# Kernel tuning notes

Hardware: AMD Instinct MI355X
Metric: run time of the kernel (lower is better)

## Reference

```python
import jax, jax.numpy as jnp
import numpy as np

N = 100000          # nodes
E = 1600000         # edges (avg degree 16)
DIN = 64
DOUT = 64
EXPERTS = 3
GATE_C = 4
TEMP = 101.0        # batch=0 < decay_lim: 100 - 0 + final_temperature(1.0)


def setup_inputs() -> dict:
    key = jax.random.key(0)
    ks = jax.random.split(key, 6)
    x = jax.random.normal(ks[0], (N, DIN), dtype=jnp.float32)
    edge_index = jax.random.randint(ks[1], (2, E), 0, N, dtype=jnp.int32)
    gate_features = jax.random.normal(ks[2], (N, GATE_C), dtype=jnp.float32)
    # per-expert GCN linear weights/bias (PyG GCNConv: lin then bias)
    W = jax.random.normal(ks[3], (EXPERTS, DIN, DOUT), dtype=jnp.float32) / np.sqrt(DIN).astype(np.float32)
    b = jnp.zeros((EXPERTS, DOUT), dtype=jnp.float32)
    # gating nn.Linear(gate_channels, experts, bias=False); stored as [GATE_C, EXPERTS] so y = gf @ Wg
    Wg = jax.random.normal(ks[4], (GATE_C, EXPERTS), dtype=jnp.float32) / np.sqrt(GATE_C).astype(np.float32)
    return {"x": x, "edge_index": edge_index, "gate_features": gate_features,
            "W": W, "b": b, "Wg": Wg}


def reference(x, edge_index, gate_features, W, b, Wg):
    n = x.shape[0]
    # --- GCN normalization with self-loops (PyG GCNConv defaults) ---
    loops = jnp.arange(n, dtype=edge_index.dtype)
    rows = jnp.concatenate([edge_index[0], loops])   # source nodes, [E+N]
    cols = jnp.concatenate([edge_index[1], loops])   # target nodes, [E+N]
    deg = jax.ops.segment_sum(jnp.ones(rows.shape, dtype=x.dtype), cols, num_segments=n)
    dinv = jnp.where(deg > 0, jax.lax.rsqrt(deg), 0.0)
    norm = dinv[rows] * dinv[cols]                   # [E+N]

    # --- gating network (softmax with decayed temperature) ---
    gate = jax.nn.softmax((gate_features @ Wg) / jnp.asarray(TEMP, x.dtype), axis=-1)  # [N, EXPERTS]

    # --- experts: GCN conv -> ReLU -> gate-weighted accumulation ---
    out = jnp.zeros((n, W.shape[-1]), dtype=x.dtype)
    for i in range(W.shape[0]):                      # small fixed expert count
        xw = x @ W[i]                                # [N, DOUT]
        msg = xw[rows] * norm[:, None]               # gather + scale, [E+N, DOUT]
        agg = jax.ops.segment_sum(msg, cols, num_segments=n) + b[i]
        out = out + gate[:, i:i + 1] * jax.nn.relu(agg)
    return out
```

## Files before the change

kernel.cpp:

```cpp
#include <hip/hip_runtime.h>
#include <hip/hip_bf16.h>

#define NN 100000
#define NE 1600000
#define NT 6250

#define NBUCK  511
#define BRANGE 196
#define CAPB   3584
#define CHUNK  4096
#define NCH    391

typedef __attribute__((ext_vector_type(8))) short bf16x8;
typedef __attribute__((ext_vector_type(4))) float f32x4;

__device__ inline float2 bf16x2_unpack(unsigned v) {
    float2 r;
    r.x = __uint_as_float(v << 16);
    r.y = __uint_as_float(v & 0xffff0000u);
    return r;
}
__device__ inline unsigned bf16x2_pack(float a, float b) {
    __hip_bfloat162 h2(__float2bfloat16(a), __float2bfloat16(b));
    unsigned u;
    __builtin_memcpy(&u, &h2, 4);
    return u;
}

__global__ __launch_bounds__(512) void bin_kernel(const int* __restrict__ rows,
                                                  const int* __restrict__ cols,
                                                  int* __restrict__ cur,
                                                  unsigned* __restrict__ eb) {
    __shared__ int hist[512];
    __shared__ int excl[512];
    __shared__ int lcur[512];
    __shared__ int gbase[512];
    __shared__ unsigned staged[CHUNK];
    __shared__ unsigned short bktarr[CHUNK];
    int t = threadIdx.x;
    int base = blockIdx.x * CHUNK;
    int cnt = min(CHUNK, NE - base);

    if (t < 512) hist[t] = 0;
    __syncthreads();

    int cbuf[CHUNK / 512];
    int rbuf[CHUNK / 512];
    #pragma unroll
    for (int k = 0; k < CHUNK / 512; k++) {
        int i = k * 512 + t;
        int c = (i < cnt) ? cols[base + i] : -1;
        int r = (i < cnt) ? rows[base + i] : 0;
        cbuf[k] = c;
        rbuf[k] = r;
        if (c >= 0) atomicAdd(&hist[(unsigned)c / BRANGE], 1);
    }
    __syncthreads();

    if (t < 64) {
        int carry = 0;
        #pragma unroll
        for (int k = 0; k < 8; k++) {
            int e = k * 64 + t;
            int h = hist[e];
            int inc = h;
            #pragma unroll
            for (int off = 1; off < 64; off <<= 1) {
                int v = __shfl_up(inc, off);
                if (t >= off) inc += v;
            }
            int ex = carry + inc - h;
            excl[e] = ex;
            lcur[e] = ex;
            carry += __shfl(inc, 63);
        }
    }
    __syncthreads();

    if (t < 512) {
        int h = hist[t];
        gbase[t] = h ? atomicAdd(cur + t * 16, h) : 0;
    }
    __syncthreads();

    #pragma unroll
    for (int k = 0; k < CHUNK / 512; k++) {
        int c = cbuf[k];
        if (c >= 0) {
            int bkt = (unsigned)c / BRANGE;
            int lp = atomicAdd(&lcur[bkt], 1);
            staged[lp] = ((unsigned)(c - bkt * BRANGE) << 24) | (unsigned)rbuf[k];
            bktarr[lp] = (unsigned short)bkt;
        }
    }
    __syncthreads();

    #pragma unroll
    for (int k = 0; k < CHUNK / 512; k++) {
        int i = k * 512 + t;
        if (i < cnt) {
            int bkt = bktarr[i];
            int pos = gbase[bkt] + (i - excl[bkt]);
            if (pos < CAPB) eb[(size_t)bkt * CAPB + pos] = staged[i];
        }
    }
}

__global__ __launch_bounds__(1024) void sortn_kernel(const int* __restrict__ cur,
                                                     const unsigned* __restrict__ eb,
                                                     int* __restrict__ srcs2,
                                                     int2* __restrict__ nsd) {
    __shared__ unsigned recs[CAPB];
    __shared__ unsigned srcl[CAPB];
    __shared__ int hist[256];
    __shared__ int lcur[256];
    int b = blockIdx.x, t = threadIdx.x;
    if (t < 256) hist[t] = 0;
    __syncthreads();
    int cnt = min(cur[b * 16], CAPB);
    const unsigned* seg = eb + (size_t)b * CAPB;
    for (int i = t; i < cnt; i += 1024) {
        unsigned r = seg[i];
        recs[i] = r;
        atomicAdd(&hist[r >> 24], 1);
    }
    __syncthreads();
    if (t < 64) {
        int e = t * 4;
        int h0 = hist[e], h1 = hist[e + 1], h2 = hist[e + 2], h3 = hist[e + 3];
        int lsum = h0 + h1 + h2 + h3;
        int inc = lsum;
        #pragma unroll
        for (int off = 1; off < 64; off <<= 1) {
            int v = __shfl_up(inc, off);
            if (t >= off) inc += v;
        }
        int ex = inc - lsum;
        int e0 = ex, e1 = ex + h0, e2 = e1 + h1, e3 = e2 + h2;
        lcur[e] = e0; lcur[e + 1] = e1; lcur[e + 2] = e2; lcur[e + 3] = e3;
        int n = b * BRANGE + e;
        if (e     < BRANGE && n     < NN) nsd[n]     = make_int2(e0, h0);
        if (e + 1 < BRANGE && n + 1 < NN) nsd[n + 1] = make_int2(e1, h1);
        if (e + 2 < BRANGE && n + 2 < NN) nsd[n + 2] = make_int2(e2, h2);
        if (e + 3 < BRANGE && n + 3 < NN) nsd[n + 3] = make_int2(e3, h3);
    }
    __syncthreads();
    for (int i = t; i < cnt; i += 1024) {
        unsigned r = recs[i];
        int p = atomicAdd(&lcur[r >> 24], 1);
        srcl[p] = r & 0xFFFFFFu;
    }
    __syncthreads();
    for (int i = t; i < cnt; i += 1024)
        srcs2[(size_t)b * CAPB + i] = (int)srcl[i];
}

__global__ __launch_bounds__(256) void xscale_kernel(const float* __restrict__ x,
                                                     const int2* __restrict__ nsd,
                                                     unsigned* __restrict__ xs) {
    int i = blockIdx.x * 256 + threadIdx.x;
    int n = i >> 5;
    int d = (i & 31) * 2;
    float2 v = *(const float2*)(x + (size_t)n * 64 + d);
    float dv = rsqrtf((float)(nsd[n].y + 1));
    xs[i] = bf16x2_pack(v.x * dv, v.y * dv);
}

__global__ void wpack_kernel(const float* __restrict__ W, __hip_bfloat16* __restrict__ Bp) {
    int idx = blockIdx.x * 256 + threadIdx.x;
    if (idx >= 12288) return;
    int j    = idx & 7;
    int lane = (idx >> 3) & 63;
    int rest = idx >> 9;
    int t    = rest % 12;
    int kh   = rest / 12;
    int k    = kh * 32 + (lane >> 4) * 8 + j;
    int col  = t * 16 + (lane & 15);
    int i    = col >> 6;
    int d    = col & 63;
    Bp[idx] = __float2bfloat16(W[(i * 64 + k) * 64 + d]);
}

__global__ __launch_bounds__(256) void gmm_kernel(const int* __restrict__ srcs2,
                                                  const int2* __restrict__ nsd,
                                                  const unsigned* __restrict__ xs,
                                                  const short* __restrict__ Bp,
                                                  const float* __restrict__ bias,
                                                  const float* __restrict__ gf,
                                                  const float* __restrict__ Wg,
                                                  float* __restrict__ out) {
    __shared__ unsigned atile[16][32];
    int lane = threadIdx.x & 63;
    int wave = threadIdx.x >> 6;
    int g  = lane >> 4;
    int gl = lane & 15;
    int gb = g << 4;
    int n0 = blockIdx.x * 16;

    int nl = wave * 4 + g;
    int n = n0 + nl;
    int2 sd = nsd[n];
    int deg = sd.y;
    int bkt = (unsigned)n / BRANGE;
    const int* seg = srcs2 + (size_t)bkt * CAPB + sd.x;
    const uint2* xsv = (const uint2*)xs;

    float4 acc = make_float4(0.f, 0.f, 0.f, 0.f);
    for (int base = 0; base < deg; base += 16) {
        int idx = 0;
        if (base + gl < deg) idx = seg[base + gl];
        int s0 = __shfl(idx, gb);
        uint2 v[16];
        #pragma unroll
        for (int j = 0; j < 16; j++) {
            int s = __shfl(idx, gb + j);
            s = (base + j < deg) ? s : s0;
            v[j] = xsv[(size_t)s * 16 + gl];
        }
        #pragma unroll
        for (int j = 0; j < 16; j++) {
            if (base + j < deg) {
                float2 f0 = bf16x2_unpack(v[j].x);
                float2 f1 = bf16x2_unpack(v[j].y);
                acc.x += f0.x; acc.y += f0.y;
                acc.z += f1.x; acc.w += f1.y;
            }
        }
    }
    uint2 svu = xsv[(size_t)n * 16 + gl];
    float2 sv0 = bf16x2_unpack(svu.x);
    float2 sv1 = bf16x2_unpack(svu.y);
    float dn = rsqrtf((float)(deg + 1));
    uint2 o;
    o.x = bf16x2_pack((acc.x + sv0.x) * dn, (acc.y + sv0.y) * dn);
    o.y = bf16x2_pack((acc.z + sv1.x) * dn, (acc.w + sv1.y) * dn);
    ((uint2*)atile[nl])[gl] = o;
    __syncthreads();

    int m = lane & 15, quad = lane >> 4;
    int dpos = wave;
    const bf16x8* arow = (const bf16x8*)atile[m];
    bf16x8 a0 = arow[quad];
    bf16x8 a1 = arow[quad + 4];

    f32x4 ce[3];
    #pragma unroll
    for (int e = 0; e < 3; e++) ce[e] = (f32x4)(0.0f);
    #pragma unroll
    for (int kh = 0; kh < 2; kh++) {
        bf16x8 a = kh ? a1 : a0;
        #pragma unroll
        for (int e = 0; e < 3; e++) {
            bf16x8 bf = *(const bf16x8*)(Bp + ((size_t)((kh * 12 + e * 4 + dpos) * 64 + lane)) * 8);
            ce[e] = __builtin_amdgcn_mfma_f32_16x16x32_bf16(a, bf, ce[e], 0, 0, 0);
        }
    }

    float wg[12];
    #pragma unroll
    for (int k = 0; k < 12; k++) wg[k] = Wg[k];

    int d = dpos * 16 + m;
    float b0 = bias[0 * 64 + d], b1 = bias[1 * 64 + d], b2 = bias[2 * 64 + d];
    #pragma unroll
    for (int reg = 0; reg < 4; reg++) {
        int nn = n0 + quad * 4 + reg;
        float4 gv = ((const float4*)gf)[nn];
        float l0 = (gv.x*wg[0] + gv.y*wg[3] + gv.z*wg[6] + gv.w*wg[9])  * (1.0f/101.0f);
        float l1 = (gv.x*wg[1] + gv.y*wg[4] + gv.z*wg[7] + gv.w*wg[10]) * (1.0f/101.0f);
        float l2 = (gv.x*wg[2] + gv.y*wg[5] + gv.z*wg[8] + gv.w*wg[11]) * (1.0f/101.0f);
        float mx = fmaxf(l0, fmaxf(l1, l2));
        float e0 = __expf(l0 - mx), e1 = __expf(l1 - mx), e2 = __expf(l2 - mx);
        float inv = 1.0f / (e0 + e1 + e2);
        float v0 = ce[0][reg] + b0;
        float v1 = ce[1][reg] + b1;
        float v2 = ce[2][reg] + b2;
        float ov = (e0 * fmaxf(v0, 0.f) + e1 * fmaxf(v1, 0.f) + e2 * fmaxf(v2, 0.f)) * inv;
        out[(size_t)nn * 64 + d] = ov;
    }
}

extern "C" void kernel_launch(void* const* d_in, const int* in_sizes, int n_in,
                              void* d_out, int out_size, void* d_ws, size_t ws_size,
                              hipStream_t stream) {
    const float* x  = (const float*)d_in[0];
    const int*   ei = (const int*)d_in[1];
    const float* gf = (const float*)d_in[2];
    const float* W  = (const float*)d_in[3];
    const float* b  = (const float*)d_in[4];
    const float* Wg = (const float*)d_in[5];
    float* out = (float*)d_out;
    const int* rows = ei;
    const int* cols = ei + NE;

    char* ws = (char*)d_ws;
    size_t off = 0;
    auto alloc = [&](size_t bytes) {
        char* p = ws + off;
        off = (off + bytes + 255) & ~(size_t)255;
        return p;
    };
    int*            cur   = (int*)alloc(512 * 16 * 4);
    unsigned*       eb    = (unsigned*)alloc((size_t)NBUCK * CAPB * 4);
    int*            srcs2 = (int*)alloc((size_t)NBUCK * CAPB * 4);
    int2*           nsd   = (int2*)alloc((size_t)NN * 8);
    unsigned*       xs    = (unsigned*)alloc((size_t)NN * 32 * 4);
    __hip_bfloat16* Bp    = (__hip_bfloat16*)alloc(12288 * 2);

    hipMemsetAsync(cur, 0, 512 * 16 * 4, stream);

    bin_kernel<<<NCH, 512, 0, stream>>>(rows, cols, cur, eb);
    sortn_kernel<<<NBUCK, 1024, 0, stream>>>(cur, eb, srcs2, nsd);
    xscale_kernel<<<NN * 32 / 256, 256, 0, stream>>>(x, nsd, xs);
    wpack_kernel<<<48, 256, 0, stream>>>(W, Bp);
    gmm_kernel<<<NT, 256, 0, stream>>>(srcs2, nsd, xs, (const short*)Bp, b, gf, Wg, out);
}
```

Before: 165.6 us.

## Replace atomic bucket offset allocation with deterministic histogram-scan-scatter passes

Splits the single binning kernel into three passes: a per-chunk histogram kernel, a scan kernel that computes per-chunk bucket base offsets and bucket totals, and a scatter kernel that uses those precomputed bases. This removes the global atomicAdd contention on bucket cursors and the memset. It also makes the edge ordering within buckets deterministic. In exchange it reads the cols array twice, adds two kernel launches and writes two NCH×512 intermediate arrays.

```diff
diff --git a/kernel.cpp b/kernel.cpp
--- a/kernel.cpp
+++ b/kernel.cpp
@@ -27,10 +27,57 @@
     return u;
 }
 
-__global__ __launch_bounds__(512) void bin_kernel(const int* __restrict__ rows,
-                                                  const int* __restrict__ cols,
-                                                  int* __restrict__ cur,
-                                                  unsigned* __restrict__ eb) {
+__global__ __launch_bounds__(512) void binA_kernel(const int* __restrict__ cols,
+                                                   int* __restrict__ hist_g) {
+    __shared__ int hist[512];
+    int t = threadIdx.x;
+    int base = blockIdx.x * CHUNK;
+    int cnt = min(CHUNK, NE - base);
+    hist[t] = 0;
+    __syncthreads();
+    #pragma unroll
+    for (int k = 0; k < CHUNK / 512; k++) {
+        int i = k * 512 + t;
+        if (i < cnt) atomicAdd(&hist[(unsigned)cols[base + i] / BRANGE], 1);
+    }
+    __syncthreads();
+    hist_g[blockIdx.x * 512 + t] = hist[t];
+}
+
+__global__ __launch_bounds__(512) void scank_kernel(const int* __restrict__ hist_g,
+                                                    int* __restrict__ gb,
+                                                    int* __restrict__ cur) {
+    int t = threadIdx.x;
+    int b = blockIdx.x * 16 + (t >> 5);
+    int l = t & 31;
+    int k0 = l * 13;
+    int h[13];
+    int s = 0;
+    #pragma unroll
+    for (int i = 0; i < 13; i++) {
+        int k = k0 + i;
+        h[i] = (k < NCH) ? hist_g[k * 512 + b] : 0;
+        s += h[i];
+    }
+    int inc = s;
+    #pragma unroll
+    for (int off = 1; off < 32; off <<= 1) {
+        int v = __shfl_up(inc, off);
+        if (l >= off) inc += v;
+    }
+    int run = inc - s;
+    #pragma unroll
+    for (int i = 0; i < 13; i++) {
+        int k = k0 + i;
+        if (k < NCH) { gb[k * 512 + b] = run; run += h[i]; }
+    }
+    if (l == 31) cur[b * 16] = inc;
+}
+
+__global__ __launch_bounds__(512) void binB_kernel(const int* __restrict__ rows,
+                                                   const int* __restrict__ cols,
+                                                   const int* __restrict__ gb,
+                                                   unsigned* __restrict__ eb) {
     __shared__ int hist[512];
     __shared__ int excl[512];
     __shared__ int lcur[512];
@@ -41,7 +88,8 @@
     int base = blockIdx.x * CHUNK;
     int cnt = min(CHUNK, NE - base);
 
-    if (t < 512) hist[t] = 0;
+    hist[t] = 0;
+    gbase[t] = gb[blockIdx.x * 512 + t];
     __syncthreads();
 
     int cbuf[CHUNK / 512];
@@ -74,12 +122,6 @@
             lcur[e] = ex;
             carry += __shfl(inc, 63);
         }
-    }
-    __syncthreads();
-
-    if (t < 512) {
-        int h = hist[t];
-        gbase[t] = h ? atomicAdd(cur + t * 16, h) : 0;
     }
     __syncthreads();
 
@@ -301,15 +343,17 @@
         return p;
     };
     int*            cur   = (int*)alloc(512 * 16 * 4);
+    int*            histg = (int*)alloc((size_t)NCH * 512 * 4);
+    int*            gbg   = (int*)alloc((size_t)NCH * 512 * 4);
     unsigned*       eb    = (unsigned*)alloc((size_t)NBUCK * CAPB * 4);
     int*            srcs2 = (int*)alloc((size_t)NBUCK * CAPB * 4);
     int2*           nsd   = (int2*)alloc((size_t)NN * 8);
     unsigned*       xs    = (unsigned*)alloc((size_t)NN * 32 * 4);
     __hip_bfloat16* Bp    = (__hip_bfloat16*)alloc(12288 * 2);
 
-    hipMemsetAsync(cur, 0, 512 * 16 * 4, stream);
-
-    bin_kernel<<<NCH, 512, 0, stream>>>(rows, cols, cur, eb);
+    binA_kernel<<<NCH, 512, 0, stream>>>(cols, histg);
+    scank_kernel<<<32, 512, 0, stream>>>(histg, gbg, cur);
+    binB_kernel<<<NCH, 512, 0, stream>>>(rows, cols, gbg, eb);
     sortn_kernel<<<NBUCK, 1024, 0, stream>>>(cur, eb, srcs2, nsd);
     xscale_kernel<<<NN * 32 / 256, 256, 0, stream>>>(x, nsd, xs);
     wpack_kernel<<<48, 256, 0, stream>>>(W, Bp);
```

New measurement: 164.0 us. No clear change (-1.0%).
